# Kernel optimization log

Hardware: AMD Instinct MI355X
Metric: run time of the kernel (lower is better)

## Reference

```python
import jax, jax.numpy as jnp
import numpy as np

B, S, D, H = 4, 2048, 1024, 16
HD = D // H  # head size = 64


def setup_inputs() -> dict:
    key = jax.random.key(0)
    ks = jax.random.split(key, 9)
    scale = 1.0 / np.sqrt(D)
    x = jax.random.normal(ks[0], (B, S, D), dtype=jnp.float32)
    Wq = jax.random.normal(ks[1], (D, D), dtype=jnp.float32) * scale
    Wk = jax.random.normal(ks[2], (D, D), dtype=jnp.float32) * scale
    Wv = jax.random.normal(ks[3], (D, D), dtype=jnp.float32) * scale
    Wo = jax.random.normal(ks[4], (D, D), dtype=jnp.float32) * scale
    bq = jax.random.normal(ks[5], (D,), dtype=jnp.float32) * 0.01
    bk = jax.random.normal(ks[6], (D,), dtype=jnp.float32) * 0.01
    bv = jax.random.normal(ks[7], (D,), dtype=jnp.float32) * 0.01
    bo = jax.random.normal(ks[8], (D,), dtype=jnp.float32) * 0.01
    return {"x": x, "Wq": Wq, "bq": bq, "Wk": Wk, "bk": bk,
            "Wv": Wv, "bv": bv, "Wo": Wo, "bo": bo}


def reference(x, Wq, bq, Wk, bk, Wv, bv, Wo, bo):
    Bv, Sv, Dv = x.shape
    # QKV projections (torch Linear: x @ W^T + b; here W stored as [in, out])
    q = x @ Wq + bq  # [B,S,D]
    k = x @ Wk + bk
    v = x @ Wv + bv
    # split heads -> [B,H,S,HD]
    q = q.reshape(Bv, Sv, H, HD).transpose(0, 2, 1, 3)
    k = k.reshape(Bv, Sv, H, HD).transpose(0, 2, 1, 3)
    v = v.reshape(Bv, Sv, H, HD).transpose(0, 2, 1, 3)
    # scaled scores + additive causal mask (upper triangle -> -inf)
    scores = jnp.einsum('bhqd,bhkd->bhqk', q, k) * (1.0 / np.sqrt(HD))
    causal = jnp.triu(jnp.full((Sv, Sv), -jnp.inf, dtype=scores.dtype), k=1)
    attn = jax.nn.softmax(scores + causal, axis=-1)
    # dropout is identity in eval / p=0
    out = jnp.einsum('bhqk,bhkd->bhqd', attn, v)
    out = out.transpose(0, 2, 1, 3).reshape(Bv, Sv, Dv)
    return out @ Wo + bo
```

## Files before the change

### kernel.cpp

```cpp
#include <hip/hip_runtime.h>
#include <hip/hip_bf16.h>


typedef unsigned short u16;
typedef short bf16x8 __attribute__((ext_vector_type(8)));
typedef float f32x4 __attribute__((ext_vector_type(4)));

constexpr int NB = 4, NS = 2048, ND = 1024, NH = 16, NHD = 64;
constexpr int NM = NB * NS;
constexpr float NEG = -1e30f;
constexpr int PAD = 68;
constexpr int EPAD = 136;

__device__ __forceinline__ u16 f2bf(float f) {
  union { float f; unsigned int u; } c; c.f = f;
  unsigned int r = (c.u + 0x7FFFu + ((c.u >> 16) & 1u)) >> 16;
  return (u16)r;
}
__device__ __forceinline__ unsigned int pk2bf(float a, float b) {
  float2 t; t.x = a; t.y = b;
  __hip_bfloat162 h = __float22bfloat162_rn(t);
  unsigned int u; __builtin_memcpy(&u, &h, 4); return u;
}
__device__ __forceinline__ void g2lds16(const u16* g, u16* l) {
  __builtin_amdgcn_global_load_lds(
      (const __attribute__((address_space(1))) void*)g,
      (__attribute__((address_space(3))) void*)l, 16, 0, 0);
}
__device__ __forceinline__ bf16x8 ldsw(const u16* b, int row, int cq) {
  return *(const bf16x8*)&b[row * 64 + ((cq ^ (row & 7)) << 3)];
}

__global__ __launch_bounds__(256) void fill_kernel(float* __restrict__ p, float v, int n) {
  int i = blockIdx.x * 256 + threadIdx.x;
  if (i < n) p[i] = v;
}

__global__ __launch_bounds__(256) void cvt_kernel(const float* __restrict__ in,
                                                  u16* __restrict__ out, int n4) {
  int i = blockIdx.x * 256 + threadIdx.x;
  if (i < n4) {
    float4 f = ((const float4*)in)[i];
    ushort4 o;
    o.x = f2bf(f.x); o.y = f2bf(f.y); o.z = f2bf(f.z); o.w = f2bf(f.w);
    ((ushort4*)out)[i] = o;
  }
}

__global__ __launch_bounds__(256) void wt_kernel(
    const float* __restrict__ s0, const float* __restrict__ s1,
    const float* __restrict__ s2, const float* __restrict__ s3,
    u16* __restrict__ d0, u16* __restrict__ d1,
    u16* __restrict__ d2, u16* __restrict__ d3) {
  const int z = blockIdx.z;
  const float* S = (z == 0) ? s0 : (z == 1) ? s1 : (z == 2) ? s2 : s3;
  u16* D = (z == 0) ? d0 : (z == 1) ? d1 : (z == 2) ? d2 : d3;
  __shared__ u16 t[64][68];
  const int r0 = blockIdx.x * 64, c0 = blockIdx.y * 64;
  const int tid = threadIdx.x;
#pragma unroll
  for (int i = 0; i < 4; i++) {
    int row = (tid >> 4) + i * 16;
    int col = (tid & 15) * 4;
    float4 f = *(const float4*)&S[(long)(r0 + row) * ND + c0 + col];
    ushort4 u; u.x = f2bf(f.x); u.y = f2bf(f.y); u.z = f2bf(f.z); u.w = f2bf(f.w);
    *(ushort4*)&t[row][col] = u;
  }
  __syncthreads();
#pragma unroll
  for (int i = 0; i < 4; i++) {
    int nrow = (tid >> 4) + i * 16;
    int kcol = (tid & 15) * 4;
    ushort4 u;
    u.x = t[kcol + 0][nrow]; u.y = t[kcol + 1][nrow];
    u.z = t[kcol + 2][nrow]; u.w = t[kcol + 3][nrow];
    *(ushort4*)&D[(long)(c0 + nrow) * ND + r0 + kcol] = u;
  }
}

__global__ __launch_bounds__(256, 3) void gemm_qkv_kernel(
    const float* __restrict__ Xf, const u16* __restrict__ Xb,
    const u16* __restrict__ WtQ,
    const float* __restrict__ bqp, const float* __restrict__ bkp,
    const float* __restrict__ bvp,
    u16* __restrict__ Qw, u16* __restrict__ Kw, u16* __restrict__ Vtw,
    int xmode) {
  __shared__ __attribute__((aligned(16))) u16 SMEM[128 * EPAD];
  u16* Asm = SMEM;
  u16* Bsm = SMEM + 8192;
  const int m0 = blockIdx.x * 128;
  const int ng = blockIdx.y;
  const int mat = ng >> 3, n0 = (ng & 7) * 128;
  const u16* Wt = WtQ + (long)mat * ND * ND;
  const int tid = threadIdx.x;
  const int w = tid >> 6, lane = tid & 63, quad = lane >> 4, lr = lane & 15;
  const int wm = w & 1, wn = w >> 1;
  const int b_r = lane >> 3, b_c = lane & 7;

  f32x4 acc[4][4] = {};

  for (int k0 = 0; k0 < ND; k0 += 64) {
    __syncthreads();
    if (xmode == 0) {
#pragma unroll
      for (int j = 0; j < 4; j++) {
        int r = w * 32 + j * 8 + b_r;
        const float* src = Xf + (long)(m0 + r) * ND + k0 + ((b_c ^ (r & 7)) << 3);
        float4 f0 = *(const float4*)src;
        float4 f1 = *(const float4*)(src + 4);
        uint4 d;
        d.x = pk2bf(f0.x, f0.y); d.y = pk2bf(f0.z, f0.w);
        d.z = pk2bf(f1.x, f1.y); d.w = pk2bf(f1.z, f1.w);
        *(uint4*)&Asm[r * 64 + (b_c << 3)] = d;
      }
    } else {
#pragma unroll
      for (int j = 0; j < 4; j++) {
        int R0 = w * 32 + j * 8;
        int r = R0 + b_r;
        g2lds16(Xb + (long)(m0 + r) * ND + k0 + ((b_c ^ (r & 7)) << 3),
                &Asm[R0 * 64]);
      }
    }
#pragma unroll
    for (int j = 0; j < 4; j++) {
      int R0 = w * 32 + j * 8;
      int r = R0 + b_r;
      g2lds16(Wt + (long)(n0 + r) * ND + k0 + ((b_c ^ (r & 7)) << 3),
              &Bsm[R0 * 64]);
    }
    __syncthreads();

#pragma unroll
    for (int kk = 0; kk < 2; kk++) {
      bf16x8 af[4], bfr[4];
#pragma unroll
      for (int mt = 0; mt < 4; mt++)
        af[mt] = ldsw(Asm, wm * 64 + mt * 16 + lr, kk * 4 + quad);
#pragma unroll
      for (int nt = 0; nt < 4; nt++)
        bfr[nt] = ldsw(Bsm, wn * 64 + nt * 16 + lr, kk * 4 + quad);
#pragma unroll
      for (int nt = 0; nt < 4; nt++)
#pragma unroll
        for (int mt = 0; mt < 4; mt++)
          acc[nt][mt] = __builtin_amdgcn_mfma_f32_16x16x32_bf16(
              af[mt], bfr[nt], acc[nt][mt], 0, 0, 0);
    }
  }

  const float* bias = (mat == 0) ? bqp : (mat == 1) ? bkp : bvp;
  __syncthreads();
  if (mat < 2) {
#pragma unroll
    for (int nt = 0; nt < 4; nt++) {
      int n_loc = wn * 64 + nt * 16 + lr;
      float bn = bias[n0 + n_loc];
#pragma unroll
      for (int mt = 0; mt < 4; mt++)
#pragma unroll
        for (int r = 0; r < 4; r++) {
          int m_loc = wm * 64 + mt * 16 + quad * 4 + r;
          SMEM[m_loc * EPAD + n_loc] = f2bf(acc[nt][mt][r] + bn);
        }
    }
    __syncthreads();
    u16* Yv = (mat == 0) ? Qw : Kw;
#pragma unroll
    for (int pass = 0; pass < 8; pass++) {
      int row = pass * 16 + (tid >> 4), c = tid & 15;
      uint4 d = *(const uint4*)&SMEM[row * EPAD + c * 8];
      int n_g = n0 + c * 8, h_ = n_g >> 6, hd_ = n_g & (NHD - 1);
      int m = m0 + row, b_ = m >> 11, s_ = m & (NS - 1);
      *(uint4*)&Yv[((long)((b_ * NH + h_) * NS + s_)) * NHD + hd_] = d;
    }
  } else {
#pragma unroll
    for (int nt = 0; nt < 4; nt++) {
      int n_loc = wn * 64 + nt * 16 + lr;
      float bn = bias[n0 + n_loc];
#pragma unroll
      for (int mt = 0; mt < 4; mt++) {
        int m_base = wm * 64 + mt * 16 + quad * 4;
        uint2 d;
        d.x = pk2bf(acc[nt][mt][0] + bn, acc[nt][mt][1] + bn);
        d.y = pk2bf(acc[nt][mt][2] + bn, acc[nt][mt][3] + bn);
        *(uint2*)&SMEM[n_loc * EPAD + m_base] = d;
      }
    }
    __syncthreads();
#pragma unroll
    for (int pass = 0; pass < 8; pass++) {
      int plane = pass * 16 + (tid >> 4), mc = tid & 15;
      uint4 d = *(const uint4*)&SMEM[plane * EPAD + mc * 8];
      int n_g = n0 + plane, h_ = n_g >> 6, hd_ = n_g & (NHD - 1);
      int m = m0 + mc * 8, b_ = m >> 11, s_ = m & (NS - 1);
      *(uint4*)&Vtw[((long)((b_ * NH + h_) * NHD + hd_)) * NS + s_] = d;
    }
  }
}

__global__ __launch_bounds__(256, 3) void gemm_out_kernel(
    const u16* __restrict__ Xg, const u16* __restrict__ Wt,
    const float* __restrict__ bias, float* __restrict__ Y) {
  __shared__ __attribute__((aligned(16))) u16 Asm[128 * 64];
  __shared__ __attribute__((aligned(16))) u16 Bsm[128 * 64];
  const int m0 = blockIdx.x * 128, n0 = blockIdx.y * 128;
  const int tid = threadIdx.x;
  const int w = tid >> 6, lane = tid & 63, quad = lane >> 4, lr = lane & 15;
  const int wm = w & 1, wn = w >> 1;
  const int b_r = lane >> 3, b_c = lane & 7;

  f32x4 acc[4][4] = {};

  for (int k0 = 0; k0 < ND; k0 += 64) {
    __syncthreads();
    const int h_ = k0 >> 6;
#pragma unroll
    for (int j = 0; j < 4; j++) {
      int R0 = w * 32 + j * 8;
      int r = R0 + b_r;
      int mrow = m0 + r, b_ = mrow >> 11, s_ = mrow & (NS - 1);
      g2lds16(Xg + ((long)((b_ * NH + h_) * NS + s_)) * NHD + ((b_c ^ (r & 7)) << 3),
              &Asm[R0 * 64]);
      g2lds16(Wt + (long)(n0 + r) * ND + k0 + ((b_c ^ (r & 7)) << 3),
              &Bsm[R0 * 64]);
    }
    __syncthreads();

#pragma unroll
    for (int kk = 0; kk < 2; kk++) {
      bf16x8 af[4], bfr[4];
#pragma unroll
      for (int mt = 0; mt < 4; mt++)
        af[mt] = ldsw(Asm, wm * 64 + mt * 16 + lr, kk * 4 + quad);
#pragma unroll
      for (int nt = 0; nt < 4; nt++)
        bfr[nt] = ldsw(Bsm, wn * 64 + nt * 16 + lr, kk * 4 + quad);
#pragma unroll
      for (int nt = 0; nt < 4; nt++)
#pragma unroll
        for (int mt = 0; mt < 4; mt++)
          acc[nt][mt] = __builtin_amdgcn_mfma_f32_16x16x32_bf16(
              af[mt], bfr[nt], acc[nt][mt], 0, 0, 0);
    }
  }

#pragma unroll
  for (int nt = 0; nt < 4; nt++) {
    int n = n0 + wn * 64 + nt * 16 + lr;
    float bn = bias[n];
#pragma unroll
    for (int mt = 0; mt < 4; mt++) {
#pragma unroll
      for (int r = 0; r < 4; r++) {
        int m = m0 + wm * 64 + mt * 16 + quad * 4 + r;
        Y[(long)m * ND + n] = acc[nt][mt][r] + bn;
      }
    }
  }
}

__global__ __launch_bounds__(512) void attn_kernel(
    u16* __restrict__ Q, const u16* __restrict__ K, const u16* __restrict__ Vtg) {
  __shared__ __attribute__((aligned(16))) u16 Klds[64 * PAD];
  __shared__ __attribute__((aligned(16))) u16 Vt[64 * PAD];
  const int bh = blockIdx.x;
  const int qt = 15 - blockIdx.y;
  const int q0 = qt * 128;
  const int tid = threadIdx.x;
  const int w = tid >> 6, lane = tid & 63, quad = lane >> 4, lr = lane & 15;
  u16* Qb = Q + (long)bh * NS * NHD;
  const u16* Kb = K + (long)bh * NS * NHD;
  const u16* Vb = Vtg + (long)bh * NHD * NS;

  const int qw0 = q0 + w * 16;
  bf16x8 qf[2];
  {
    int m = qw0 + lr;
    qf[0] = *(const bf16x8*)&Qb[(long)m * NHD + quad * 8];
    qf[1] = *(const bf16x8*)&Qb[(long)m * NHD + 32 + quad * 8];
  }
  const bf16x8 ones = {0x3F80, 0x3F80, 0x3F80, 0x3F80,
                       0x3F80, 0x3F80, 0x3F80, 0x3F80};

  f32x4 oaccT[4] = {};
  f32x4 lacc = {};

  const int srow = tid >> 3, sa = tid & 7;
  const int vcb = (sa >> 2) * 32 + ((sa & 1) << 4) + (((sa >> 1) & 1) << 2);
  const float kexp = 0.125f * 1.4426950408889634f;
  const int jmax = q0 + 64;

  for (int j0 = 0; j0 <= jmax; j0 += 64) {
    __syncthreads();
    *(uint4*)&Klds[srow * PAD + sa * 8] =
        *(const uint4*)&Kb[(long)(j0 + srow) * NHD + sa * 8];
    {
      uint4 v = *(const uint4*)&Vb[(long)srow * NS + j0 + sa * 8];
      uint2 v01; v01.x = v.x; v01.y = v.y;
      uint2 v23; v23.x = v.z; v23.y = v.w;
      *(uint2*)&Vt[srow * PAD + vcb] = v01;
      *(uint2*)&Vt[srow * PAD + vcb + 8] = v23;
    }
    __syncthreads();

    if (j0 > qw0 + 15) continue;

    f32x4 scT[4] = {};
#pragma unroll
    for (int t = 0; t < 4; t++) {
      bf16x8 kf0 = *(bf16x8*)&Klds[(t * 16 + lr) * PAD + quad * 8];
      bf16x8 kf1 = *(bf16x8*)&Klds[(t * 16 + lr) * PAD + 32 + quad * 8];
      scT[t] = __builtin_amdgcn_mfma_f32_16x16x32_bf16(kf0, qf[0], scT[t], 0, 0, 0);
      scT[t] = __builtin_amdgcn_mfma_f32_16x16x32_bf16(kf1, qf[1], scT[t], 0, 0, 0);
    }

    if (j0 + 63 > qw0) {
#pragma unroll
      for (int t = 0; t < 4; t++)
#pragma unroll
        for (int r = 0; r < 4; r++)
          if ((j0 + t * 16 + quad * 4 + r) > (qw0 + lr)) scT[t][r] = NEG;
    }

#pragma unroll
    for (int t = 0; t < 4; t++)
#pragma unroll
      for (int r = 0; r < 4; r++) scT[t][r] = exp2f(scT[t][r] * kexp);

#pragma unroll
    for (int kk = 0; kk < 2; kk++) {
      uint4 pu;
      pu.x = pk2bf(scT[2 * kk][0], scT[2 * kk][1]);
      pu.y = pk2bf(scT[2 * kk][2], scT[2 * kk][3]);
      pu.z = pk2bf(scT[2 * kk + 1][0], scT[2 * kk + 1][1]);
      pu.w = pk2bf(scT[2 * kk + 1][2], scT[2 * kk + 1][3]);
      bf16x8 pt; __builtin_memcpy(&pt, &pu, 16);
      lacc = __builtin_amdgcn_mfma_f32_16x16x32_bf16(ones, pt, lacc, 0, 0, 0);
#pragma unroll
      for (int dt = 0; dt < 4; dt++) {
        bf16x8 va = *(bf16x8*)&Vt[(dt * 16 + lr) * PAD + kk * 32 + quad * 8];
        oaccT[dt] = __builtin_amdgcn_mfma_f32_16x16x32_bf16(va, pt, oaccT[dt], 0, 0, 0);
      }
    }
  }

  const float inv = 1.0f / lacc[0];
#pragma unroll
  for (int dt = 0; dt < 4; dt++) {
    uint2 o;
    o.x = pk2bf(oaccT[dt][0] * inv, oaccT[dt][1] * inv);
    o.y = pk2bf(oaccT[dt][2] * inv, oaccT[dt][3] * inv);
    *(uint2*)&Qb[(long)(qw0 + lr) * NHD + dt * 16 + quad * 4] = o;
  }
}

extern "C" void kernel_launch(void* const* d_in, const int* in_sizes, int n_in,
                              void* d_out, int out_size, void* d_ws, size_t ws_size,
                              hipStream_t stream) {
  const float* x  = (const float*)d_in[0];
  const float* Wq = (const float*)d_in[1];
  const float* bq = (const float*)d_in[2];
  const float* Wk = (const float*)d_in[3];
  const float* bk = (const float*)d_in[4];
  const float* Wv = (const float*)d_in[5];
  const float* bv = (const float*)d_in[6];
  const float* Wo = (const float*)d_in[7];
  const float* bo = (const float*)d_in[8];

  const size_t BUF = (size_t)NM * ND * sizeof(u16);
  if (ws_size < 2 * BUF) {
    fill_kernel<<<(out_size + 255) / 256, 256, 0, stream>>>((float*)d_out, 0.f, out_size);
    return;
  }

  u16* Qw  = (u16*)d_ws;
  u16* Vtw = Qw + (long)NM * ND;
  u16* Kw  = (u16*)d_out;
  u16* WtQ = Kw + (long)NM * ND;
  u16* WtO = WtQ + 3L * ND * ND;
  const bool bigws = ws_size >= 3 * BUF;
  u16* Xb = bigws ? (Vtw + (long)NM * ND) : nullptr;

  wt_kernel<<<dim3(16, 16, 4), 256, 0, stream>>>(Wq, Wk, Wv, Wo,
      WtQ, WtQ + (long)ND * ND, WtQ + 2L * ND * ND, WtO);
  if (bigws)
    cvt_kernel<<<(NM * ND / 4 + 255) / 256, 256, 0, stream>>>(x, Xb, NM * ND / 4);

  gemm_qkv_kernel<<<dim3(64, 24), 256, 0, stream>>>(
      x, Xb, WtQ, bq, bk, bv, Qw, Kw, Vtw, bigws ? 2 : 0);
  attn_kernel<<<dim3(NB * NH, NS / 128), 512, 0, stream>>>(Qw, Kw, Vtw);
  hipMemcpyAsync(Vtw, WtO, (size_t)ND * ND * sizeof(u16),
                 hipMemcpyDeviceToDevice, stream);
  gemm_out_kernel<<<dim3(64, 8), 256, 0, stream>>>(Qw, Vtw, bo, (float*)d_out);
}
```

Baseline: 244.3 us.

## Fold softmax scale into Q weights, pre-permute V, use direct global-to-LDS loads in attention

Q weights and bias are pre-scaled by 0.125*log2(e) during weight conversion, so the attention kernel can apply a raw exp2 without a multiply. The QKV epilogue writes V^T with the column permutation the attention kernel previously applied in shared memory. This lets attention stage K and V tiles through global_load_lds with an XOR swizzle instead of register round trips and padded LDS. Scaling Q in bf16 before the GEMM slightly changes rounding, and the attention kernel now depends on the permuted V layout written by the QKV epilogue.

```diff
diff --git a/kernel.cpp b/kernel.cpp
--- a/kernel.cpp
+++ b/kernel.cpp
@@ -9,8 +9,14 @@
 constexpr int NB = 4, NS = 2048, ND = 1024, NH = 16, NHD = 64;
 constexpr int NM = NB * NS;
 constexpr float NEG = -1e30f;
-constexpr int PAD = 68;
 constexpr int EPAD = 136;
+constexpr float KEXP = 0.125f * 1.4426950408889634f;
+
+#if __has_builtin(__builtin_amdgcn_exp2f)
+#define EXP2(x) __builtin_amdgcn_exp2f(x)
+#else
+#define EXP2(x) exp2f(x)
+#endif
 
 __device__ __forceinline__ u16 f2bf(float f) {
   union { float f; unsigned int u; } c; c.f = f;
@@ -55,6 +61,7 @@
   const int z = blockIdx.z;
   const float* S = (z == 0) ? s0 : (z == 1) ? s1 : (z == 2) ? s2 : s3;
   u16* D = (z == 0) ? d0 : (z == 1) ? d1 : (z == 2) ? d2 : d3;
+  const float sc = (z == 0) ? KEXP : 1.0f;
   __shared__ u16 t[64][68];
   const int r0 = blockIdx.x * 64, c0 = blockIdx.y * 64;
   const int tid = threadIdx.x;
@@ -63,7 +70,9 @@
     int row = (tid >> 4) + i * 16;
     int col = (tid & 15) * 4;
     float4 f = *(const float4*)&S[(long)(r0 + row) * ND + c0 + col];
-    ushort4 u; u.x = f2bf(f.x); u.y = f2bf(f.y); u.z = f2bf(f.z); u.w = f2bf(f.w);
+    ushort4 u;
+    u.x = f2bf(f.x * sc); u.y = f2bf(f.y * sc);
+    u.z = f2bf(f.z * sc); u.w = f2bf(f.w * sc);
     *(ushort4*)&t[row][col] = u;
   }
   __syncthreads();
@@ -150,12 +159,13 @@
   }
 
   const float* bias = (mat == 0) ? bqp : (mat == 1) ? bkp : bvp;
+  const float bsc = (mat == 0) ? KEXP : 1.0f;
   __syncthreads();
   if (mat < 2) {
 #pragma unroll
     for (int nt = 0; nt < 4; nt++) {
       int n_loc = wn * 64 + nt * 16 + lr;
-      float bn = bias[n0 + n_loc];
+      float bn = bias[n0 + n_loc] * bsc;
 #pragma unroll
       for (int mt = 0; mt < 4; mt++)
 #pragma unroll
@@ -195,7 +205,13 @@
       uint4 d = *(const uint4*)&SMEM[plane * EPAD + mc * 8];
       int n_g = n0 + plane, h_ = n_g >> 6, hd_ = n_g & (NHD - 1);
       int m = m0 + mc * 8, b_ = m >> 11, s_ = m & (NS - 1);
-      *(uint4*)&Vtw[((long)((b_ * NH + h_) * NHD + hd_)) * NS + s_] = d;
+      long base = ((long)((b_ * NH + h_) * NHD + hd_)) * NS;
+      int cb = s_ & ~31;
+      int s1 = (mc & 1) * 16 + ((mc >> 1) & 1) * 4;
+      uint2 lo; lo.x = d.x; lo.y = d.y;
+      uint2 hi; hi.x = d.z; hi.y = d.w;
+      *(uint2*)&Vtw[base + cb + s1] = lo;
+      *(uint2*)&Vtw[base + cb + s1 + 8] = hi;
     }
   }
 }
@@ -263,8 +279,8 @@
 
 __global__ __launch_bounds__(512) void attn_kernel(
     u16* __restrict__ Q, const u16* __restrict__ K, const u16* __restrict__ Vtg) {
-  __shared__ __attribute__((aligned(16))) u16 Klds[64 * PAD];
-  __shared__ __attribute__((aligned(16))) u16 Vt[64 * PAD];
+  __shared__ __attribute__((aligned(16))) u16 Klds[64 * 64];
+  __shared__ __attribute__((aligned(16))) u16 Vt[64 * 64];
   const int bh = blockIdx.x;
   const int qt = 15 - blockIdx.y;
   const int q0 = qt * 128;
@@ -287,22 +303,15 @@
   f32x4 oaccT[4] = {};
   f32x4 lacc = {};
 
-  const int srow = tid >> 3, sa = tid & 7;
-  const int vcb = (sa >> 2) * 32 + ((sa & 1) << 4) + (((sa >> 1) & 1) << 2);
-  const float kexp = 0.125f * 1.4426950408889634f;
+  const int sr = lane >> 3;
+  const int ssw = (((lane & 7) ^ sr) << 3);
+  const int krow0 = w * 8;
   const int jmax = q0 + 64;
 
   for (int j0 = 0; j0 <= jmax; j0 += 64) {
     __syncthreads();
-    *(uint4*)&Klds[srow * PAD + sa * 8] =
-        *(const uint4*)&Kb[(long)(j0 + srow) * NHD + sa * 8];
-    {
-      uint4 v = *(const uint4*)&Vb[(long)srow * NS + j0 + sa * 8];
-      uint2 v01; v01.x = v.x; v01.y = v.y;
-      uint2 v23; v23.x = v.z; v23.y = v.w;
-      *(uint2*)&Vt[srow * PAD + vcb] = v01;
-      *(uint2*)&Vt[srow * PAD + vcb + 8] = v23;
-    }
+    g2lds16(Kb + (long)(j0 + krow0 + sr) * NHD + ssw, &Klds[krow0 * 64]);
+    g2lds16(Vb + (long)(krow0 + sr) * NS + j0 + ssw, &Vt[krow0 * 64]);
     __syncthreads();
 
     if (j0 > qw0 + 15) continue;
@@ -310,8 +319,9 @@
     f32x4 scT[4] = {};
 #pragma unroll
     for (int t = 0; t < 4; t++) {
-      bf16x8 kf0 = *(bf16x8*)&Klds[(t * 16 + lr) * PAD + quad * 8];
-      bf16x8 kf1 = *(bf16x8*)&Klds[(t * 16 + lr) * PAD + 32 + quad * 8];
+      int kr = t * 16 + lr;
+      bf16x8 kf0 = ldsw(Klds, kr, quad);
+      bf16x8 kf1 = ldsw(Klds, kr, 4 + quad);
       scT[t] = __builtin_amdgcn_mfma_f32_16x16x32_bf16(kf0, qf[0], scT[t], 0, 0, 0);
       scT[t] = __builtin_amdgcn_mfma_f32_16x16x32_bf16(kf1, qf[1], scT[t], 0, 0, 0);
     }
@@ -327,7 +337,7 @@
 #pragma unroll
     for (int t = 0; t < 4; t++)
 #pragma unroll
-      for (int r = 0; r < 4; r++) scT[t][r] = exp2f(scT[t][r] * kexp);
+      for (int r = 0; r < 4; r++) scT[t][r] = EXP2(scT[t][r]);
 
 #pragma unroll
     for (int kk = 0; kk < 2; kk++) {
@@ -340,7 +350,7 @@
       lacc = __builtin_amdgcn_mfma_f32_16x16x32_bf16(ones, pt, lacc, 0, 0, 0);
 #pragma unroll
       for (int dt = 0; dt < 4; dt++) {
-        bf16x8 va = *(bf16x8*)&Vt[(dt * 16 + lr) * PAD + kk * 32 + quad * 8];
+        bf16x8 va = ldsw(Vt, dt * 16 + lr, kk * 4 + quad);
         oaccT[dt] = __builtin_amdgcn_mfma_f32_16x16x32_bf16(va, pt, oaccT[dt], 0, 0, 0);
       }
     }
```

Measured after the change: 230.4 us. 5.7% less time.
